# Performance work log

Measured on AMD Instinct MI355X. Metric: run time of the kernel, lower is better.

## Reference

```python
import jax, jax.numpy as jnp
import numpy as np

B, N, D, H, O, K, N_USER, C = 1, 4096, 64, 4, 64, 2, 4000, 2


def setup_inputs() -> dict:
    key = jax.random.key(0)
    ks = jax.random.split(key, 7)
    h = jax.random.normal(ks[0], (B, N, D), jnp.float32)
    # dense 0/1 adjacency per heterogeneous kind, with self-loops so no row is empty
    adj = jax.random.randint(ks[1], (K, B, N, N), 0, 2).astype(jnp.float32)
    hadj = jnp.maximum(adj, jnp.eye(N, dtype=jnp.float32))
    s = 1.0 / np.sqrt(D).astype(np.float32)
    w = jax.random.normal(ks[2], (K, H, D, O), jnp.float32) * s
    a_src = jax.random.normal(ks[3], (K, H, O, 1), jnp.float32) * (1.0 / np.sqrt(O).astype(np.float32))
    a_dst = jax.random.normal(ks[4], (K, H, O, 1), jnp.float32) * (1.0 / np.sqrt(O).astype(np.float32))
    fc_w = jax.random.normal(ks[5], (C, O * K), jnp.float32) * (1.0 / np.sqrt(O * K).astype(np.float32))
    fc_b = jnp.zeros((C,), jnp.float32)
    return {"h": h, "hadj": hadj, "w": w, "a_src": a_src, "a_dst": a_dst, "fc_w": fc_w, "fc_b": fc_b}


def _gat(h, adj, w_k, a_src_k, a_dst_k):
    # h: (B,N,D); adj: (B,N,N); w_k: (H,D,O); a_*: (H,O,1)
    h_prime = jnp.einsum('bnf,hfo->bhno', h, w_k)          # (B,H,N,O)
    t = jnp.tanh(h_prime)
    attn_src = jnp.einsum('bhno,hoi->bhni', t, a_src_k)    # (B,H,N,1)
    attn_dst = jnp.einsum('bhno,hoi->bhni', t, a_dst_k)    # (B,H,N,1)
    attn = attn_src + jnp.swapaxes(attn_dst, -1, -2)       # (B,H,N,N) broadcast add
    attn = jnp.where(attn >= 0, attn, 0.2 * attn)          # LeakyReLU(0.2)
    attn = jnp.where(adj[:, None] > 0, attn, -jnp.inf)     # dense mask
    attn = jax.nn.softmax(attn, axis=-1)                   # dropout is a no-op in eval
    out = jnp.einsum('bhnm,bhmo->bhno', attn, h_prime)     # (B,H,N,O)
    return out.mean(axis=1)                                # mean over heads -> (B,N,O)


def reference(h, hadj, w, a_src, a_dst, fc_w, fc_b):
    embs = []
    for k in range(K):  # small fixed loop over heterogeneous node kinds
        x = _gat(h, hadj[k], w[k], a_src[k], a_dst[k])
        embs.append(x[:, :N_USER])
    type_aware = jnp.concatenate(embs, axis=-1)            # (B, N_USER, K*O)
    logits = type_aware @ fc_w.T + fc_b                    # (B, N_USER, C)
    return jax.nn.log_softmax(logits, axis=-1)
```

## Files before the change

### kernel.cpp

```cpp
#include <hip/hip_runtime.h>
#include <math.h>

constexpr int KK = 2;
constexpr int HH = 4;
constexpr int NN = 4096;
constexpr int DD = 64;
constexpr int OO = 64;
constexpr int NU = 4000;
constexpr int CC = 2;
constexpr int JSPLIT = 16;
constexpr int JCHUNK = NN / JSPLIT;
constexpr float LOG2E = 1.44269504088896340736f;

typedef float vf4 __attribute__((ext_vector_type(4)));
typedef float vf2 __attribute__((ext_vector_type(2)));

__device__ __forceinline__ float fexp2(float x) {
#if __has_builtin(__builtin_amdgcn_exp2f)
  return __builtin_amdgcn_exp2f(x);
#else
  return exp2f(x);
#endif
}
__device__ __forceinline__ float frcp(float x) {
#if __has_builtin(__builtin_amdgcn_rcpf)
  return __builtin_amdgcn_rcpf(x);
#else
  return 1.0f / x;
#endif
}
__device__ __forceinline__ float ftanh(float x) {
  float e = fexp2(x * (2.0f * LOG2E));
  return 1.0f - 2.0f * frcp(e + 1.0f);
}

__global__ __launch_bounds__(256) void gat_phase1(
    const float* __restrict__ hsrc, const float* __restrict__ w,
    const float* __restrict__ a_src, const float* __restrict__ a_dst,
    const float* __restrict__ fc_w,
    float* __restrict__ Ap, float* __restrict__ A5p,
    float* __restrict__ Bp, float* __restrict__ B5p,
    float* __restrict__ G0p, float* __restrict__ G1p) {
  const int kh = blockIdx.y;
  const int k = kh >> 2;
  const int i0 = blockIdx.x * 64;
  const int tid = threadIdx.x;

  __shared__ float h_s[DD][68];
  __shared__ float w_s[DD][OO];
  __shared__ float part[4][64][17];

  {
    const vf4* wp = (const vf4*)(w + (size_t)kh * DD * OO);
    vf4* ws4 = (vf4*)w_s;
    for (int t = tid; t < DD * OO / 4; t += 256) ws4[t] = wp[t];
  }
  for (int t = tid; t < 1024; t += 256) {
    const int row = t >> 4;
    const int f4 = (t & 15) * 4;
    vf4 v = *(const vf4*)(hsrc + (size_t)(i0 + row) * DD + f4);
    h_s[f4 + 0][row] = v.x;
    h_s[f4 + 1][row] = v.y;
    h_s[f4 + 2][row] = v.z;
    h_s[f4 + 3][row] = v.w;
  }
  __syncthreads();

  const int og = tid & 15;
  const int rg = tid >> 4;
  const int o0 = og * 4;
  const int r0 = rg * 4;

  float hp[4][4];
#pragma unroll
  for (int j = 0; j < 4; ++j)
#pragma unroll
    for (int u = 0; u < 4; ++u) hp[j][u] = 0.0f;

#pragma unroll 8
  for (int f = 0; f < DD; ++f) {
    vf4 hv = *(const vf4*)&h_s[f][r0];
    vf4 wv = *(const vf4*)&w_s[f][o0];
    hp[0][0] = fmaf(hv.x, wv.x, hp[0][0]);
    hp[0][1] = fmaf(hv.x, wv.y, hp[0][1]);
    hp[0][2] = fmaf(hv.x, wv.z, hp[0][2]);
    hp[0][3] = fmaf(hv.x, wv.w, hp[0][3]);
    hp[1][0] = fmaf(hv.y, wv.x, hp[1][0]);
    hp[1][1] = fmaf(hv.y, wv.y, hp[1][1]);
    hp[1][2] = fmaf(hv.y, wv.z, hp[1][2]);
    hp[1][3] = fmaf(hv.y, wv.w, hp[1][3]);
    hp[2][0] = fmaf(hv.z, wv.x, hp[2][0]);
    hp[2][1] = fmaf(hv.z, wv.y, hp[2][1]);
    hp[2][2] = fmaf(hv.z, wv.z, hp[2][2]);
    hp[2][3] = fmaf(hv.z, wv.w, hp[2][3]);
    hp[3][0] = fmaf(hv.w, wv.x, hp[3][0]);
    hp[3][1] = fmaf(hv.w, wv.y, hp[3][1]);
    hp[3][2] = fmaf(hv.w, wv.z, hp[3][2]);
    hp[3][3] = fmaf(hv.w, wv.w, hp[3][3]);
  }

  float as[4], ad[4], f0[4], f1[4];
#pragma unroll
  for (int u = 0; u < 4; ++u) {
    as[u] = a_src[kh * OO + o0 + u];
    ad[u] = a_dst[kh * OO + o0 + u];
    f0[u] = fc_w[0 * (KK * OO) + k * OO + o0 + u];
    f1[u] = fc_w[1 * (KK * OO) + k * OO + o0 + u];
  }

#pragma unroll
  for (int j = 0; j < 4; ++j) {
    float sp = 0.0f, dp = 0.0f, g0 = 0.0f, g1 = 0.0f;
#pragma unroll
    for (int u = 0; u < 4; ++u) {
      float v = hp[j][u];
      float t = ftanh(v);
      sp = fmaf(t, as[u], sp);
      dp = fmaf(t, ad[u], dp);
      g0 = fmaf(v, f0[u], g0);
      g1 = fmaf(v, f1[u], g1);
    }
    part[0][r0 + j][og] = sp;
    part[1][r0 + j][og] = dp;
    part[2][r0 + j][og] = g0;
    part[3][r0 + j][og] = g1;
  }
  __syncthreads();

  {
    const int val = tid >> 6;
    const int j2 = tid & 63;
    const float* pr = &part[val][j2][0];
    vf4 s0 = *(const vf4*)(pr + 0);
    vf4 s1 = *(const vf4*)(pr + 4);
    vf4 s2 = *(const vf4*)(pr + 8);
    vf4 s3 = *(const vf4*)(pr + 12);
    vf4 t4 = s0 + s1 + s2 + s3;
    float sum = t4.x + t4.y + t4.z + t4.w;
    const size_t idx = (size_t)kh * NN + i0 + j2;
    if (val == 0) {
      float sp = sum * LOG2E;
      Ap[idx] = fexp2(sp);
      A5p[idx] = fexp2(0.2f * sp);
    } else if (val == 1) {
      float dp = sum * LOG2E;
      Bp[idx] = fexp2(dp);
      B5p[idx] = fexp2(0.2f * dp);
    } else if (val == 2) {
      G0p[idx] = sum;
    } else {
      G1p[idx] = sum;
    }
  }
}

__global__ __launch_bounds__(256) void gat_phase2(
    const float* __restrict__ adj, const float* __restrict__ Ap,
    const float* __restrict__ A5p, const float* __restrict__ Bp,
    const float* __restrict__ B5p, const float* __restrict__ G0p,
    const float* __restrict__ G1p, float* __restrict__ P) {
  const int k = blockIdx.y >> 4;
  const int chunk = blockIdx.y & 15;
  const int r0 = blockIdx.x * 16;
  const int tid = threadIdx.x;
  const int wave = tid >> 6;
  const int lane = tid & 63;
  const int row = lane & 15;
  const int jsub = lane >> 4;
  const int i = r0 + row;
  const int j0 = chunk * JCHUNK;

  __shared__ float lds[4][HH][JCHUNK];

  {
    const float* plane_src[4] = {Bp, B5p, G0p, G1p};
    const int h = tid >> 6;
    const int pos = (tid & 63) * 4;
    const size_t gbase = (size_t)(k * HH + h) * NN + j0 + pos;
#pragma unroll
    for (int step = 0; step < 4; ++step) {
      vf4 v = *(const vf4*)(plane_src[step] + gbase);
      *(vf4*)&lds[step][h][pos] = v;
    }
  }

  vf2 Apk[4], A5pk[4];
#pragma unroll
  for (int h = 0; h < 4; ++h) {
    const size_t ia = (size_t)(k * HH + h) * NN + i;
    float a = Ap[ia];
    float a5 = A5p[ia];
    Apk[h] = (vf2){a, a};
    A5pk[h] = (vf2){a5, a5};
  }

  vf2 l2[4], a02[4], a12[4];
#pragma unroll
  for (int h = 0; h < 4; ++h) {
    l2[h] = (vf2){0.0f, 0.0f};
    a02[h] = (vf2){0.0f, 0.0f};
    a12[h] = (vf2){0.0f, 0.0f};
  }

  __syncthreads();

  const float* arow =
      adj + (size_t)k * NN * NN + (size_t)i * NN + j0 + jsub * 4;
  vf4 aj[4];
#pragma unroll
  for (int q = 0; q < 4; ++q)
    aj[q] = *(const vf4*)(arow + (wave + q * 4) * 16);

#pragma unroll
  for (int s = 0; s < 4; ++s) {
    const int t = wave + s * 4;
    const vf4 av = aj[s];
    const vf2 av01 = (vf2){av.x, av.y};
    const vf2 av23 = (vf2){av.z, av.w};
    const int jl = t * 16 + jsub * 4;
#pragma unroll
    for (int h = 0; h < 4; ++h) {
      vf4 Bv = *(const vf4*)&lds[0][h][jl];
      vf4 B5v = *(const vf4*)&lds[1][h][jl];
      vf4 G0v = *(const vf4*)&lds[2][h][jl];
      vf4 G1v = *(const vf4*)&lds[3][h][jl];

      vf2 m01 = Apk[h] * (vf2){Bv.x, Bv.y};
      vf2 n01 = A5pk[h] * (vf2){B5v.x, B5v.y};
      vf2 e01 = (vf2){fmaxf(m01.x, n01.x), fmaxf(m01.y, n01.y)};
      vf2 pa01 = e01 * av01;
      l2[h] += pa01;
      a02[h] += pa01 * (vf2){G0v.x, G0v.y};
      a12[h] += pa01 * (vf2){G1v.x, G1v.y};

      vf2 m23 = Apk[h] * (vf2){Bv.z, Bv.w};
      vf2 n23 = A5pk[h] * (vf2){B5v.z, B5v.w};
      vf2 e23 = (vf2){fmaxf(m23.x, n23.x), fmaxf(m23.y, n23.y)};
      vf2 pa23 = e23 * av23;
      l2[h] += pa23;
      a02[h] += pa23 * (vf2){G0v.z, G0v.w};
      a12[h] += pa23 * (vf2){G1v.z, G1v.w};
    }
  }

  float l[4], a0[4], a1[4];
#pragma unroll
  for (int h = 0; h < 4; ++h) {
    l[h] = l2[h].x + l2[h].y;
    a0[h] = a02[h].x + a02[h].y;
    a1[h] = a12[h].x + a12[h].y;
  }
#pragma unroll
  for (int h = 0; h < 4; ++h) {
    l[h] += __shfl_xor(l[h], 16, 64);
    l[h] += __shfl_xor(l[h], 32, 64);
    a0[h] += __shfl_xor(a0[h], 16, 64);
    a0[h] += __shfl_xor(a0[h], 32, 64);
    a1[h] += __shfl_xor(a1[h], 16, 64);
    a1[h] += __shfl_xor(a1[h], 32, 64);
  }

  __shared__ float sred[4][12][16];
  if (lane < 16) {
#pragma unroll
    for (int h = 0; h < 4; ++h) {
      sred[wave][h * 3 + 0][row] = l[h];
      sred[wave][h * 3 + 1][row] = a0[h];
      sred[wave][h * 3 + 2][row] = a1[h];
    }
  }
  __syncthreads();
  if (tid < 192) {
    const int v = tid >> 4;
    const int rr = tid & 15;
    float sum =
        sred[0][v][rr] + sred[1][v][rr] + sred[2][v][rr] + sred[3][v][rr];
    const int h = v / 3, c = v % 3;
    size_t base =
        ((((size_t)(k * JSPLIT + chunk) * HH + h) * 3 + c)) * NU + (r0 + rr);
    P[base] = sum;
  }
}

__global__ __launch_bounds__(256) void gat_phase3(
    const float* __restrict__ P, const float* __restrict__ fc_b,
    float* __restrict__ out) {
  const int tid = threadIdx.x;
  const int g = tid & 7;
  const int il = tid >> 3;
  const int i = blockIdx.x * 32 + il;
  const int k = g >> 2, h = g & 3;

  float ls = 0.0f, a0 = 0.0f, a1 = 0.0f;
#pragma unroll
  for (int ch = 0; ch < JSPLIT; ++ch) {
    size_t b = (((size_t)(k * JSPLIT + ch) * HH + h) * 3) * NU + i;
    ls += P[b];
    a0 += P[b + NU];
    a1 += P[b + 2 * (size_t)NU];
  }
  float inv = 1.0f / ls;
  float p0 = 0.25f * a0 * inv;
  float p1 = 0.25f * a1 * inv;

  p0 += __shfl_xor(p0, 1, 64);
  p0 += __shfl_xor(p0, 2, 64);
  p0 += __shfl_xor(p0, 4, 64);
  p1 += __shfl_xor(p1, 1, 64);
  p1 += __shfl_xor(p1, 2, 64);
  p1 += __shfl_xor(p1, 4, 64);

  if (g == 0) {
    float l0 = p0 + fc_b[0];
    float l1 = p1 + fc_b[1];
    float m = fmaxf(l0, l1);
    float lse = m + logf(expf(l0 - m) + expf(l1 - m));
    out[(size_t)i * CC + 0] = l0 - lse;
    out[(size_t)i * CC + 1] = l1 - lse;
  }
}

extern "C" void kernel_launch(void* const* d_in, const int* in_sizes, int n_in,
                              void* d_out, int out_size, void* d_ws, size_t ws_size,
                              hipStream_t stream) {
  const float* hsrc  = (const float*)d_in[0];
  const float* hadj  = (const float*)d_in[1];
  const float* w     = (const float*)d_in[2];
  const float* a_src = (const float*)d_in[3];
  const float* a_dst = (const float*)d_in[4];
  const float* fc_w  = (const float*)d_in[5];
  const float* fc_b  = (const float*)d_in[6];
  float* out = (float*)d_out;

  char* ws = (char*)d_ws;
  float* Ap  = (float*)(ws + 0);
  float* A5p = (float*)(ws + 131072);
  float* Bp  = (float*)(ws + 262144);
  float* B5p = (float*)(ws + 393216);
  float* G0p = (float*)(ws + 524288);
  float* G1p = (float*)(ws + 655360);
  float* P   = (float*)(ws + 786432);

  dim3 g1(NN / 64, KK * HH);
  gat_phase1<<<g1, 256, 0, stream>>>(hsrc, w, a_src, a_dst, fc_w,
                                     Ap, A5p, Bp, B5p, G0p, G1p);
  dim3 g2(NU / 16, KK * JSPLIT);
  gat_phase2<<<g2, 256, 0, stream>>>(hadj, Ap, A5p, Bp, B5p, G0p, G1p, P);
  gat_phase3<<<NU / 32, 256, 0, stream>>>(P, fc_b, out);
}
```

Measured before the change: 218.3 us.

## Halve j-split, hoist nontemporal adjacency loads, coalesce phase3 reads via LDS

Halves the number of j-chunks in phase2 so each block handles 512 columns. It issues eight nontemporal adjacency vector loads before the LDS fill and barrier, so the streaming reads overlap the staging. Phase3 now puts consecutive rows on consecutive lanes for coalesced partial reads, and reduces across head/kind groups through shared memory instead of shuffles, with a vectorised output store. The changes cut partial-sum traffic and launch parallelism but raise register and LDS use per block.

```diff
diff --git a/kernel.cpp b/kernel.cpp
--- a/kernel.cpp
+++ b/kernel.cpp
@@ -8,7 +8,7 @@
 constexpr int OO = 64;
 constexpr int NU = 4000;
 constexpr int CC = 2;
-constexpr int JSPLIT = 16;
+constexpr int JSPLIT = 8;
 constexpr int JCHUNK = NN / JSPLIT;
 constexpr float LOG2E = 1.44269504088896340736f;
 
@@ -159,8 +159,8 @@
     const float* __restrict__ A5p, const float* __restrict__ Bp,
     const float* __restrict__ B5p, const float* __restrict__ G0p,
     const float* __restrict__ G1p, float* __restrict__ P) {
-  const int k = blockIdx.y >> 4;
-  const int chunk = blockIdx.y & 15;
+  const int k = blockIdx.y >> 3;
+  const int chunk = blockIdx.y & 7;
   const int r0 = blockIdx.x * 16;
   const int tid = threadIdx.x;
   const int wave = tid >> 6;
@@ -174,15 +174,23 @@
 
   {
     const float* plane_src[4] = {Bp, B5p, G0p, G1p};
-    const int h = tid >> 6;
-    const int pos = (tid & 63) * 4;
-    const size_t gbase = (size_t)(k * HH + h) * NN + j0 + pos;
-#pragma unroll
-    for (int step = 0; step < 4; ++step) {
-      vf4 v = *(const vf4*)(plane_src[step] + gbase);
-      *(vf4*)&lds[step][h][pos] = v;
-    }
-  }
+#pragma unroll
+    for (int step = 0; step < 8; ++step) {
+      const int wi = ((step & 1) << 8) | tid;
+      const int h = wi >> 7;
+      const int pos = (wi & 127) * 4;
+      vf4 v = *(const vf4*)(plane_src[step >> 1] +
+                            (size_t)(k * HH + h) * NN + j0 + pos);
+      *(vf4*)&lds[step >> 1][h][pos] = v;
+    }
+  }
+
+  const float* arow =
+      adj + (size_t)k * NN * NN + (size_t)i * NN + j0 + jsub * 4;
+  vf4 aj[8];
+#pragma unroll
+  for (int q = 0; q < 8; ++q)
+    aj[q] = __builtin_nontemporal_load((const vf4*)(arow + (wave + q * 4) * 16));
 
   vf2 Apk[4], A5pk[4];
 #pragma unroll
@@ -204,15 +212,8 @@
 
   __syncthreads();
 
-  const float* arow =
-      adj + (size_t)k * NN * NN + (size_t)i * NN + j0 + jsub * 4;
-  vf4 aj[4];
-#pragma unroll
-  for (int q = 0; q < 4; ++q)
-    aj[q] = *(const vf4*)(arow + (wave + q * 4) * 16);
-
-#pragma unroll
-  for (int s = 0; s < 4; ++s) {
+#pragma unroll
+  for (int s = 0; s < 8; ++s) {
     const int t = wave + s * 4;
     const vf4 av = aj[s];
     const vf2 av01 = (vf2){av.x, av.y};
@@ -286,8 +287,8 @@
     const float* __restrict__ P, const float* __restrict__ fc_b,
     float* __restrict__ out) {
   const int tid = threadIdx.x;
-  const int g = tid & 7;
-  const int il = tid >> 3;
+  const int il = tid & 31;
+  const int g = tid >> 5;
   const int i = blockIdx.x * 32 + il;
   const int k = g >> 2, h = g & 3;
 
@@ -303,20 +304,23 @@
   float p0 = 0.25f * a0 * inv;
   float p1 = 0.25f * a1 * inv;
 
-  p0 += __shfl_xor(p0, 1, 64);
-  p0 += __shfl_xor(p0, 2, 64);
-  p0 += __shfl_xor(p0, 4, 64);
-  p1 += __shfl_xor(p1, 1, 64);
-  p1 += __shfl_xor(p1, 2, 64);
-  p1 += __shfl_xor(p1, 4, 64);
-
-  if (g == 0) {
-    float l0 = p0 + fc_b[0];
-    float l1 = p1 + fc_b[1];
+  __shared__ float s0[8][33], s1[8][33];
+  s0[g][il] = p0;
+  s1[g][il] = p1;
+  __syncthreads();
+
+  if (tid < 32) {
+    float l0 = fc_b[0], l1 = fc_b[1];
+#pragma unroll
+    for (int g2 = 0; g2 < 8; ++g2) {
+      l0 += s0[g2][tid];
+      l1 += s1[g2][tid];
+    }
+    const int io = blockIdx.x * 32 + tid;
     float m = fmaxf(l0, l1);
     float lse = m + logf(expf(l0 - m) + expf(l1 - m));
-    out[(size_t)i * CC + 0] = l0 - lse;
-    out[(size_t)i * CC + 1] = l1 - lse;
+    vf2 r = {l0 - lse, l1 - lse};
+    *(vf2*)(out + (size_t)io * CC) = r;
   }
 }
 
```

After: 229.3 us. +5.0%, slower.
